# Performance work log

Hardware: AMD Instinct MI355X
Metric: run time of the kernel (lower is better)

Reference implementation:

```python
import jax, jax.numpy as jnp
import numpy as np

DIM = 192
HEADS = 4
EPS = 1e-12  # F.normalize default eps


def setup_inputs() -> dict:
    key = jax.random.key(0)
    ks = jax.random.split(key, 5)
    b, c, h, w = 8, DIM, 128, 128
    x = jax.random.normal(ks[0], (b, c, h, w), dtype=jnp.float32)
    w_qkv = jax.random.normal(ks[1], (3 * DIM, DIM, 1, 1), dtype=jnp.float32) * (1.0 / np.sqrt(DIM))
    w_dw = jax.random.normal(ks[2], (3 * DIM, 1, 3, 3), dtype=jnp.float32) * (1.0 / 3.0)
    w_proj = jax.random.normal(ks[3], (DIM, DIM, 1, 1), dtype=jnp.float32) * (1.0 / np.sqrt(DIM))
    temperature = jnp.ones((HEADS, 1, 1), dtype=jnp.float32)
    return {"x": x, "w_qkv": w_qkv, "w_dw": w_dw, "w_proj": w_proj, "temperature": temperature}


def _conv1x1(x, w):
    # x: [b,c,h,w], w: [o,c,1,1] -> [b,o,h,w]
    return jnp.einsum('bchw,oc->bohw', x, w[:, :, 0, 0])


def _dwconv3x3(x, w):
    # depthwise 3x3, padding=1; x: [b,C,h,w], w: [C,1,3,3]
    C = x.shape[1]
    return jax.lax.conv_general_dilated(
        x, w, window_strides=(1, 1), padding=((1, 1), (1, 1)),
        dimension_numbers=('NCHW', 'OIHW', 'NCHW'), feature_group_count=C)


def _l2norm(x):
    n = jnp.linalg.norm(x, axis=-1, keepdims=True)
    return x / jnp.maximum(n, EPS)


def reference(x, w_qkv, w_dw, w_proj, temperature):
    b, c, h, w = x.shape
    head = HEADS
    ch = c // head  # channels per head
    qkv = _dwconv3x3(_conv1x1(x, w_qkv), w_dw)  # [b, 3c, h, w]
    q, k, v = jnp.split(qkv, 3, axis=1)  # each [b, c, h, w]

    def to_heads(t):
        # b (head ch) h w -> b head h (ch w)
        t = t.reshape(b, head, ch, h, w)
        return t.transpose(0, 1, 3, 2, 4).reshape(b, head, h, ch * w)

    q1 = _l2norm(to_heads(q))
    k1 = _l2norm(to_heads(k))
    v1 = to_heads(v)
    # attn over height dim: [b, head, h, h]
    attn = jax.nn.softmax(jnp.einsum('bhif,bhjf->bhij', q1, k1) * temperature[None], axis=-1)
    out = jnp.einsum('bhij,bhjf->bhif', attn, v1)  # [b, head, h, ch*w]
    # b head h (ch w) -> b (head ch) h w
    out = out.reshape(b, head, h, ch, w).transpose(0, 1, 3, 2, 4).reshape(b, c, h, w)
    return _conv1x1(out, w_proj)
```

## Files before the change

kernel.cpp:

```cpp
#include <hip/hip_runtime.h>
#include <hip/hip_bf16.h>

#define BB 8
#define CC 192
#define C3 576
#define NH 4
#define CH 48
#define HH 128
#define WW 128
#define HW 16384
#define FF 6144

typedef short s16x8 __attribute__((ext_vector_type(8)));
typedef float f32x4 __attribute__((ext_vector_type(4)));

constexpr size_t SPM = 32ull * 128 * 128;

constexpr size_t OFF_XT  = 0;
constexpr size_t SZ_XT   = (size_t)BB * HW * CC * 2;
constexpr size_t OFF_WQ  = OFF_XT + SZ_XT;
constexpr size_t SZ_WQ   = (size_t)C3 * CC * 2;
constexpr size_t OFF_WP  = OFF_WQ + SZ_WQ;
constexpr size_t SZ_WP   = (size_t)CC * CC * 2;
constexpr size_t OFF_RAW = OFF_WP + SZ_WP;
constexpr size_t SZ_RAW  = (size_t)BB * C3 * HW * 2;
constexpr size_t OFF_DW  = OFF_RAW + SZ_RAW;
constexpr size_t OFF_SP  = OFF_DW + SZ_RAW;
constexpr size_t OFF_ATB = OFF_SP + 8 * SPM * 4;
constexpr size_t OFF_RQ  = OFF_ATB + 32ull * 128 * 128 * 2;
constexpr size_t OFF_RK  = OFF_RQ + 32 * 128 * 4;
constexpr size_t OFF_PS  = OFF_SP;

__device__ __forceinline__ short bf16bits(float v) {
  __hip_bfloat16 t = __float2bfloat16(v);
  return *reinterpret_cast<short*>(&t);
}
__device__ __forceinline__ float b2f(short u) {
  union { unsigned int i; float f; } x;
  x.i = ((unsigned int)(unsigned short)u) << 16;
  return x.f;
}

__device__ __forceinline__ void gload16(const void* g, void* l) {
  __builtin_amdgcn_global_load_lds((const __attribute__((address_space(1))) unsigned int*)g,
                                   (__attribute__((address_space(3))) unsigned int*)l, 16, 0, 0);
}

#define VMWAIT(N) asm volatile("s_waitcnt vmcnt(" #N ")" ::: "memory")
__device__ __forceinline__ void vmdrain() { asm volatile("s_waitcnt vmcnt(0)" ::: "memory"); }
__device__ __forceinline__ void ldsbar() {
  asm volatile("s_waitcnt lgkmcnt(0)" ::: "memory");
  __builtin_amdgcn_s_barrier();
}

__global__ __launch_bounds__(256) void k_cvt_t(const float* __restrict__ in,
                                               __hip_bfloat16* __restrict__ outT) {
  const int p0 = blockIdx.x * 64;
  const int c0 = blockIdx.y * 32;
  const int b = blockIdx.z;
  __shared__ float t[32][65];
  const float* ib = in + (size_t)b * CC * HW;
  const int tid = threadIdx.x;
  {
    const int c = tid >> 3, pl = (tid & 7) * 8;
    const float* s = ib + (size_t)(c0 + c) * HW + p0 + pl;
#pragma unroll
    for (int j = 0; j < 8; ++j) t[c][pl + j] = s[j];
  }
  __syncthreads();
  {
    const int pl = tid >> 2, cl = (tid & 3) * 8;
    __hip_bfloat16* d = outT + (size_t)b * HW * CC + (size_t)(p0 + pl) * CC + c0 + cl;
#pragma unroll
    for (int j = 0; j < 8; ++j) d[j] = __float2bfloat16(t[cl + j][pl]);
  }
}

__global__ __launch_bounds__(256) void k_cvt_w2(const float* __restrict__ in1, int n1,
                                                const float* __restrict__ in2, int n2,
                                                __hip_bfloat16* __restrict__ out) {
  const int i = blockIdx.x * 256 + threadIdx.x;
  if (i < n1) out[i] = __float2bfloat16(in1[i]);
  else if (i < n1 + n2) out[i] = __float2bfloat16(in2[i - n1]);
}

__global__ __launch_bounds__(256) void k_gemm(const __hip_bfloat16* __restrict__ xT,
                                              const __hip_bfloat16* __restrict__ Wb,
                                              __hip_bfloat16* __restrict__ out) {
  const int pG = blockIdx.x * 4;
  const int mBase = blockIdx.y * 96;
  const int b = blockIdx.z;
  __shared__ char smem[62976];
  const int tid = threadIdx.x, wave = tid >> 6, lane = tid & 63;
  const int wm = wave >> 1, wn = wave & 1;
  const __hip_bfloat16* xb = xT + (size_t)b * HW * CC;
  char* Bbase = smem + 36864;

#pragma unroll
  for (int it = 0; it < 9; ++it) {
    const int s = it * 256 + tid;
    const int kc = s / 384, ci = s % 384;
    const int row = ci & 15, kg = (ci >> 4) & 3, mf = ci >> 6;
    gload16(Wb + (size_t)(mBase + mf * 16 + row) * CC + kc * 32 + kg * 8,
            smem + it * 4096 + wave * 1024);
  }

  auto stageB = [&](int pt, int kc, int buf) {
    char* Blc = Bbase + buf * 8192;
    const int pBase = (pG + pt) * 128;
#pragma unroll
    for (int is = 0; is < 2; ++is) {
      const int ci = is * 256 + tid;
      const int col = ci & 15, kg = (ci >> 4) & 3, nf = ci >> 6;
      gload16(xb + (size_t)(pBase + nf * 16 + col) * CC + kc * 32 + kg * 8,
              Blc + is * 4096 + wave * 1024);
    }
  };

  short* E = (short*)Bbase;
  const int r0 = (lane >> 4) * 4, cl = lane & 15;

  for (int pt = 0; pt < 4; ++pt) {
    stageB(pt, 0, 0);
    stageB(pt, 1, 1);
    f32x4 acc[3][4] = {};
#pragma unroll
    for (int kc = 0; kc < 6; ++kc) {
      if (kc < 4) stageB(pt, kc + 2, (kc + 2) % 3);
      if (kc < 4) VMWAIT(4);
      else if (kc == 4) VMWAIT(2);
      else VMWAIT(0);
      __builtin_amdgcn_s_barrier();
      char* Alc = smem + kc * 6144;
      char* Blc = Bbase + (kc % 3) * 8192;
      s16x8 a[3], bf[4];
#pragma unroll
      for (int i = 0; i < 3; ++i) a[i] = *(const s16x8*)(Alc + ((wm * 3 + i) << 10) + (lane << 4));
#pragma unroll
      for (int j = 0; j < 4; ++j) bf[j] = *(const s16x8*)(Blc + ((wn * 4 + j) << 10) + (lane << 4));
#pragma unroll
      for (int i = 0; i < 3; ++i)
#pragma unroll
        for (int j = 0; j < 4; ++j)
          acc[i][j] = __builtin_amdgcn_mfma_f32_16x16x32_bf16(a[i], bf[j], acc[i][j], 0, 0, 0);
      __builtin_amdgcn_s_barrier();
    }
#pragma unroll
    for (int i = 0; i < 3; ++i) {
      const int lr = wm * 48 + i * 16 + r0;
#pragma unroll
      for (int j = 0; j < 4; ++j) {
        const int col = (wn * 4 + j) * 16 + cl;
#pragma unroll
        for (int r = 0; r < 4; ++r) E[(lr + r) * 136 + col] = bf16bits(acc[i][j][r]);
      }
    }
    ldsbar();
    __hip_bfloat16* ob = out + (size_t)b * C3 * HW + (pG + pt) * 128;
#pragma unroll
    for (int it = 0; it < 6; ++it) {
      const int vi = it * 256 + tid;
      const int row = vi >> 4, c8 = (vi & 15) * 8;
      const s16x8 v = *(const s16x8*)(E + row * 136 + c8);
      *(s16x8*)(ob + (size_t)(mBase + row) * HW + c8) = v;
    }
    ldsbar();
  }
}

__global__ __launch_bounds__(256) void k_dwconv(const __hip_bfloat16* __restrict__ in,
                                                const float* __restrict__ wdw,
                                                __hip_bfloat16* __restrict__ out,
                                                __hip_bfloat16* __restrict__ vt,
                                                float* __restrict__ psum) {
  const int h0 = blockIdx.x * 32;
  const int c = blockIdx.y;
  const int b = blockIdx.z;
  __shared__ __hip_bfloat16 IN[34][152];
  __shared__ char TR[8192];
  const int tid = threadIdx.x;
  const __hip_bfloat16* src = in + ((size_t)b * C3 + c) * HW;
  if (tid < 68) {
    const int r = tid >> 1, col = (tid & 1) ? 136 : 0;
    *(s16x8*)(&IN[r][col]) = (s16x8){};
  }
#pragma unroll
  for (int it = 0; it < 3; ++it) {
    const int vi = it * 256 + tid;
    if (vi < 544) {
      const int r = vi >> 4, w8 = vi & 15;
      const int hg = h0 - 1 + r;
      s16x8 v = {};
      if (hg >= 0 && hg < HH) v = *(const s16x8*)(src + (size_t)hg * WW + w8 * 8);
      *(s16x8*)(&IN[r][8 + w8 * 8]) = v;
    }
  }
  const float* wp = wdw + c * 9;
  float wgt[9];
#pragma unroll
  for (int q = 0; q < 9; ++q) wgt[q] = wp[q];
  __syncthreads();

  const int hl = tid >> 3, w0 = (tid & 7) * 16;
  float res[16] = {};
#pragma unroll
  for (int dh = 0; dh < 3; ++dh) {
    const __hip_bfloat16* rp = &IN[hl + dh][0];
    const s16x8 v0 = *(const s16x8*)(rp + w0);
    const s16x8 v1 = *(const s16x8*)(rp + w0 + 8);
    const s16x8 v2 = *(const s16x8*)(rp + w0 + 16);
    const s16x8 v3 = *(const s16x8*)(rp + w0 + 24);
    float rv[18];
    rv[0] = b2f(v0[7]);
#pragma unroll
    for (int e = 0; e < 8; ++e) rv[1 + e] = b2f(v1[e]);
#pragma unroll
    for (int e = 0; e < 8; ++e) rv[9 + e] = b2f(v2[e]);
    rv[17] = b2f(v3[0]);
    const float wa = wgt[dh * 3], wb = wgt[dh * 3 + 1], wc = wgt[dh * 3 + 2];
#pragma unroll
    for (int ww = 0; ww < 16; ++ww)
      res[ww] += rv[ww] * wa + rv[ww + 1] * wb + rv[ww + 2] * wc;
  }
  if (c < 2 * CC) {
    short pk[16];
#pragma unroll
    for (int ww = 0; ww < 16; ++ww) pk[ww] = bf16bits(res[ww]);
    __hip_bfloat16* dst = out + ((size_t)b * C3 + c) * HW + (size_t)(h0 + hl) * WW + w0;
    *(s16x8*)dst = *(const s16x8*)pk;
    *(s16x8*)(dst + 8) = *(const s16x8*)(pk + 8);
    float ss = 0.f;
#pragma unroll
    for (int ww = 0; ww < 16; ++ww) ss += res[ww] * res[ww];
#pragma unroll
    for (int off = 4; off > 0; off >>= 1) ss += __shfl_down(ss, off);
    if ((tid & 7) == 0) psum[((size_t)b * HH + h0 + hl) * 384 + c] = ss;
  } else {
    const int rel = c - 2 * CC;
    const int hd = rel / CH, ch = rel - hd * CH;
#pragma unroll
    for (int ww = 0; ww < 16; ++ww) {
      const int w = w0 + ww;
      const int blk = ((w << 2) + (hl >> 3)) ^ ((w >> 3) & 3);
      *(short*)(TR + (blk << 4) + ((hl & 7) << 1)) = bf16bits(res[ww]);
    }
    __syncthreads();
    const int w = tid >> 1, hf = tid & 1;
    short ot[16];
#pragma unroll
    for (int j = 0; j < 2; ++j) {
      const int hh = hf * 16 + j * 8;
      const int blk = ((w << 2) + (hh >> 3)) ^ ((w >> 3) & 3);
      *(s16x8*)(ot + j * 8) = *(const s16x8*)(TR + (blk << 4));
    }
    __hip_bfloat16* vd = vt + ((size_t)(b * NH + hd) * FF + (size_t)ch * WW + w) * HH + h0 + hf * 16;
    *(s16x8*)vd = *(const s16x8*)ot;
    *(s16x8*)(vd + 8) = *(const s16x8*)(ot + 8);
  }
}

__global__ __launch_bounds__(64) void k_norms2(const float* __restrict__ psum,
                                               float* __restrict__ rq, float* __restrict__ rk) {
  const int i = blockIdx.x;
  const int hd = blockIdx.y;
  const int b = blockIdx.z & 7;
  const int which = blockIdx.z >> 3;
  const int lane = threadIdx.x;
  float s = 0.f;
  if (lane < 48) s = psum[((size_t)b * HH + i) * 384 + which * CC + hd * CH + lane];
#pragma unroll
  for (int off = 32; off > 0; off >>= 1) s += __shfl_down(s, off);
  if (lane == 0) {
    const float n = sqrtf(s);
    float* dst = which ? rk : rq;
    dst[(b * NH + hd) * HH + i] = 1.f / fmaxf(n, 1e-12f);
  }
}

__global__ __launch_bounds__(256) void k_qkm(const __hip_bfloat16* __restrict__ dw,
                                             float* __restrict__ sp) {
  const int ks = blockIdx.x;
  const int bh = blockIdx.y;
  const int b = bh >> 2, hd = bh & 3;
  const __hip_bfloat16* qb = dw + ((size_t)b * C3 + hd * CH) * HW;
  const __hip_bfloat16* kb = dw + ((size_t)b * C3 + CC + hd * CH) * HW;
  __shared__ char smem[49152];
  const int tid = threadIdx.x, wave = tid >> 6, lane = tid & 63;
  const int wm = wave >> 1, wn = wave & 1;
  f32x4 acc[4][4] = {};

  auto stage = [&](int chunk, int buf) {
    const int ch = ks * 6 + (chunk >> 2);
    const int w0 = (chunk & 3) * 32;
    char* Alc = smem + buf * 16384;
    char* Blc = Alc + 8192;
#pragma unroll
    for (int is = 0; is < 2; ++is) {
      const int ci = is * 256 + tid;
      const int row = ci & 15, kg = (ci >> 4) & 3, mf = ci >> 6;
      gload16(qb + (size_t)ch * HW + (mf * 16 + row) * WW + w0 + kg * 8,
              Alc + is * 4096 + wave * 1024);
    }
#pragma unroll
    for (int is = 0; is < 2; ++is) {
      const int ci = is * 256 + tid;
      const int col = ci & 15, kg = (ci >> 4) & 3, nf = ci >> 6;
      gload16(kb + (size_t)ch * HW + (nf * 16 + col) * WW + w0 + kg * 8,
              Blc + is * 4096 + wave * 1024);
    }
  };

  stage(0, 0);
  stage(1, 1);
  for (int chunk = 0; chunk < 24; ++chunk) {
    if (chunk < 22) stage(chunk + 2, (chunk + 2) % 3);
    if (chunk < 22) VMWAIT(8);
    else if (chunk == 22) VMWAIT(4);
    else VMWAIT(0);
    __builtin_amdgcn_s_barrier();
    char* Alc = smem + (chunk % 3) * 16384;
    char* Blc = Alc + 8192;
    s16x8 a[4], bf[4];
#pragma unroll
    for (int i = 0; i < 4; ++i) a[i] = *(const s16x8*)(Alc + ((wm * 4 + i) << 10) + (lane << 4));
#pragma unroll
    for (int j = 0; j < 4; ++j) bf[j] = *(const s16x8*)(Blc + ((wn * 4 + j) << 10) + (lane << 4));
#pragma unroll
    for (int i = 0; i < 4; ++i)
#pragma unroll
      for (int j = 0; j < 4; ++j)
        acc[i][j] = __builtin_amdgcn_mfma_f32_16x16x32_bf16(a[i], bf[j], acc[i][j], 0, 0, 0);
    __builtin_amdgcn_s_barrier();
  }
  float* o = sp + (size_t)ks * SPM + (size_t)bh * HH * HH;
  const int r0 = (lane >> 4) * 4, cl = lane & 15;
#pragma unroll
  for (int i = 0; i < 4; ++i)
#pragma unroll
    for (int j = 0; j < 4; ++j) {
      const int ii = wm * 64 + i * 16 + r0;
      const int jj = wn * 64 + j * 16 + cl;
#pragma unroll
      for (int r = 0; r < 4; ++r) o[(ii + r) * HH + jj] = acc[i][j][r];
    }
}

__global__ __launch_bounds__(256) void k_softmax(const float* __restrict__ sp,
                                                 const float* __restrict__ rq,
                                                 const float* __restrict__ rk,
                                                 const float* __restrict__ temp,
                                                 __hip_bfloat16* __restrict__ atb) {
  const int wave = threadIdx.x >> 6, lane = threadIdx.x & 63;
  const int i = blockIdx.x * 4 + wave;
  const int bh = blockIdx.y;
  const int hd = bh & 3;
  const size_t rowoff = ((size_t)bh * HH + i) * HH;
  float s0 = 0.f, s1 = 0.f;
#pragma unroll
  for (int ks = 0; ks < 8; ++ks) {
    s0 += sp[ks * SPM + rowoff + lane];
    s1 += sp[ks * SPM + rowoff + lane + 64];
  }
  const float scale = rq[bh * HH + i] * temp[hd];
  s0 *= scale * rk[bh * HH + lane];
  s1 *= scale * rk[bh * HH + lane + 64];
  float m = fmaxf(s0, s1);
#pragma unroll
  for (int off = 32; off > 0; off >>= 1) m = fmaxf(m, __shfl_xor(m, off));
  const float e0 = expf(s0 - m), e1 = expf(s1 - m);
  float ssum = e0 + e1;
#pragma unroll
  for (int off = 32; off > 0; off >>= 1) ssum += __shfl_xor(ssum, off);
  const float inv = 1.f / ssum;
  atb[rowoff + lane] = __float2bfloat16(e0 * inv);
  atb[rowoff + lane + 64] = __float2bfloat16(e1 * inv);
}

__global__ __launch_bounds__(256) void k_pvm(const __hip_bfloat16* __restrict__ atb,
                                             const __hip_bfloat16* __restrict__ vt,
                                             __hip_bfloat16* __restrict__ pvout) {
  const int fs0 = blockIdx.x * 2;
  const int bh = blockIdx.y;
  const __hip_bfloat16* ab = atb + (size_t)bh * HH * HH;
  __shared__ char smem[57344];
  const int tid = threadIdx.x, wave = tid >> 6, lane = tid & 63;
  const int wm = wave >> 1, wn = wave & 1;

#pragma unroll
  for (int it = 0; it < 8; ++it) {
    const int s = it * 256 + tid;
    const int kc = s >> 9, ci = s & 511;
    const int row = ci & 15, kg = (ci >> 4) & 3, mf = ci >> 6;
    gload16(ab + (size_t)(mf * 16 + row) * HH + kc * 32 + kg * 8,
            smem + it * 4096 + wave * 1024);
  }
  char* Bbase = smem + 32768;

  auto stageB = [&](int st, int buf) {
    const int fs = fs0 + (st >> 2);
    const int kj0 = (st & 3) * 32;
    const __hip_bfloat16* vb = vt + ((size_t)bh * FF + fs * 128) * HH;
    char* Blc = Bbase + buf * 8192;
#pragma unroll
    for (int is = 0; is < 2; ++is) {
      const int ci = is * 256 + tid;
      const int col = ci & 15, kg = (ci >> 4) & 3, nf = ci >> 6;
      gload16(vb + (size_t)(nf * 16 + col) * HH + kj0 + kg * 8,
              Blc + is * 4096 + wave * 1024);
    }
  };

  stageB(0, 0);
  stageB(1, 1);
  const int r0 = (lane >> 4) * 4, cl = lane & 15;
  for (int fr = 0; fr < 2; ++fr) {
    f32x4 acc[4][4] = {};
#pragma unroll
    for (int kc = 0; kc < 4; ++kc) {
      const int st = fr * 4 + kc;
      if (st < 6) stageB(st + 2, (st + 2) % 3);
      if (st < 6) VMWAIT(4);
      else if (st == 6) VMWAIT(2);
      else VMWAIT(0);
      __builtin_amdgcn_s_barrier();
      char* Alc = smem + kc * 8192;
      char* Blc = Bbase + (st % 3) * 8192;
      s16x8 a[4], bf[4];
#pragma unroll
      for (int i = 0; i < 4; ++i) a[i] = *(const s16x8*)(Alc + ((wm * 4 + i) << 10) + (lane << 4));
#pragma unroll
      for (int j = 0; j < 4; ++j) bf[j] = *(const s16x8*)(Blc + ((wn * 4 + j) << 10) + (lane << 4));
#pragma unroll
      for (int i = 0; i < 4; ++i)
#pragma unroll
        for (int j = 0; j < 4; ++j)
          acc[i][j] = __builtin_amdgcn_mfma_f32_16x16x32_bf16(a[i], bf[j], acc[i][j], 0, 0, 0);
      __builtin_amdgcn_s_barrier();
    }
    __hip_bfloat16* ob = pvout + (size_t)bh * HH * FF;
    const int fs = fs0 + fr;
#pragma unroll
    for (int i = 0; i < 4; ++i)
#pragma unroll
      for (int j = 0; j < 4; ++j) {
        const int ii = wm * 64 + i * 16 + r0;
        const int f = fs * 128 + (wn * 4 + j) * 16 + cl;
#pragma unroll
        for (int r = 0; r < 4; ++r) ob[(size_t)(ii + r) * FF + f] = __float2bfloat16(acc[i][j][r]);
      }
  }
}

__global__ __launch_bounds__(256) void k_proj(const __hip_bfloat16* __restrict__ pv,
                                              const __hip_bfloat16* __restrict__ Wp,
                                              float* __restrict__ out) {
  const int i = blockIdx.x;
  const int b = blockIdx.y;
  __shared__ __hip_bfloat16 Al[6144];
  __shared__ __hip_bfloat16 Braw[12288];
  __shared__ __hip_bfloat16 Bfrag[4096];
  char* Alc = (char*)Al;
  char* Brc = (char*)Braw;
  char* Bfc = (char*)Bfrag;
  const int tid = threadIdx.x, wave = tid >> 6, lane = tid & 63;
  const int wm = wave >> 1, wn = wave & 1;
  f32x4 acc[6][4] = {};
  for (int hf = 0; hf < 2; ++hf) {
    if (hf) __syncthreads();
#pragma unroll
    for (int it = 0; it < 6; ++it) {
      const int vi = it * 256 + tid;
      const int r = vi >> 4, w8 = vi & 15;
      const int hi = (r >= 48) ? 1 : 0;
      const int hd = hf * 2 + hi, ch = r - hi * 48;
      const s16x8 v = *(const s16x8*)(pv + ((size_t)(b * NH + hd) * HH + i) * FF + ch * 128 + w8 * 8);
      *(s16x8*)(Brc + r * 256 + ((w8 ^ (r & 15)) << 4)) = v;
    }
    __syncthreads();
    for (int kc = 0; kc < 3; ++kc) {
      const int c0 = hf * 96 + kc * 32;
#pragma unroll
      for (int is = 0; is < 3; ++is) {
        const int ci = is * 256 + tid;
        const int row = ci & 15, kg = (ci >> 4) & 3, mf = ci >> 6;
        gload16(Wp + (size_t)(mf * 16 + row) * CC + c0 + kg * 8,
                Alc + is * 4096 + wave * 1024);
      }
#pragma unroll
      for (int it = 0; it < 2; ++it) {
        const int vi = it * 256 + tid;
        const int col = vi & 15, kg = (vi >> 4) & 3, nf = vi >> 6;
        const int w = nf * 16 + col;
        short tmp[8];
#pragma unroll
        for (int e = 0; e < 8; ++e) {
          const int r = (kc * 4 + kg) * 8 + e;
          tmp[e] = *(const short*)(Brc + r * 256 + (((w >> 3) ^ (r & 15)) << 4) + (w & 7) * 2);
        }
        *(s16x8*)(Bfc + ((nf * 64 + kg * 16 + col) << 4)) = *(const s16x8*)tmp;
      }
      vmdrain();
      __syncthreads();
      s16x8 a[6], bf[4];
#pragma unroll
      for (int mi = 0; mi < 6; ++mi)
        a[mi] = *(const s16x8*)(Alc + ((wm * 6 + mi) << 10) + (lane << 4));
#pragma unroll
      for (int j = 0; j < 4; ++j)
        bf[j] = *(const s16x8*)(Bfc + (((wn * 4 + j) * 64 + lane) << 4));
#pragma unroll
      for (int mi = 0; mi < 6; ++mi)
#pragma unroll
        for (int j = 0; j < 4; ++j)
          acc[mi][j] = __builtin_amdgcn_mfma_f32_16x16x32_bf16(a[mi], bf[j], acc[mi][j], 0, 0, 0);
      __syncthreads();
    }
  }
  const int r0 = (lane >> 4) * 4, cl = lane & 15;
#pragma unroll
  for (int mi = 0; mi < 6; ++mi) {
    const int o = (wm * 6 + mi) * 16 + r0;
#pragma unroll
    for (int j = 0; j < 4; ++j) {
      const int w = (wn * 4 + j) * 16 + cl;
      float* dst = out + ((size_t)b * CC + o) * HW + i * 128 + w;
#pragma unroll
      for (int r = 0; r < 4; ++r) dst[(size_t)r * HW] = acc[mi][j][r];
    }
  }
}

extern "C" void kernel_launch(void* const* d_in, const int* in_sizes, int n_in,
                              void* d_out, int out_size, void* d_ws, size_t ws_size,
                              hipStream_t stream) {
  const float* x     = (const float*)d_in[0];
  const float* wqkv  = (const float*)d_in[1];
  const float* wdw   = (const float*)d_in[2];
  const float* wproj = (const float*)d_in[3];
  const float* temp  = (const float*)d_in[4];

  char* ws = (char*)d_ws;
  __hip_bfloat16* xTb    = (__hip_bfloat16*)(ws + OFF_XT);
  __hip_bfloat16* vt     = (__hip_bfloat16*)(ws + OFF_XT);
  __hip_bfloat16* Wq     = (__hip_bfloat16*)(ws + OFF_WQ);
  __hip_bfloat16* Wp     = (__hip_bfloat16*)(ws + OFF_WP);
  __hip_bfloat16* qkvraw = (__hip_bfloat16*)(ws + OFF_RAW);
  __hip_bfloat16* pvout  = (__hip_bfloat16*)(ws + OFF_RAW);
  __hip_bfloat16* qkvdw  = (__hip_bfloat16*)(ws + OFF_DW);
  float* sp    = (float*)(ws + OFF_SP);
  float* psum  = (float*)(ws + OFF_PS);
  __hip_bfloat16* atb = (__hip_bfloat16*)(ws + OFF_ATB);
  float* rq    = (float*)(ws + OFF_RQ);
  float* rk    = (float*)(ws + OFF_RK);

  k_cvt_w2<<<dim3((C3 * CC + CC * CC + 255) / 256), 256, 0, stream>>>(wqkv, C3 * CC, wproj, CC * CC, Wq);
  k_cvt_t<<<dim3(HW / 64, CC / 32, BB), 256, 0, stream>>>(x, xTb);
  k_gemm<<<dim3(HW / 512, C3 / 96, BB), 256, 0, stream>>>(xTb, Wq, qkvraw);
  k_dwconv<<<dim3(HH / 32, C3, BB), 256, 0, stream>>>(qkvraw, wdw, qkvdw, vt, psum);
  k_norms2<<<dim3(HH, NH, 2 * BB), 64, 0, stream>>>(psum, rq, rk);
  k_qkm<<<dim3(8, 32), 256, 0, stream>>>(qkvdw, sp);
  k_softmax<<<dim3(HH / 4, 32), 256, 0, stream>>>(sp, rq, rk, temp, atb);
  k_pvm<<<dim3(24, 32), 256, 0, stream>>>(atb, vt, pvout);
  k_proj<<<dim3(HH, BB), 256, 0, stream>>>(pvout, Wp, (float*)d_out);
}
```

Measured before the change: 253.3 us.

## Loop dwconv over height tiles with register prefetch; split QK^T GEMM rows

The depthwise conv kernel now processes all four 32-row height tiles of a channel in one block, double-buffering shared memory and prefetching the next tile into registers while computing the current one. It launches 4x fewer blocks and overlaps global loads with compute. The QK^T kernel is split along the query-row dimension into two 64-row halves, which doubles its grid from 256 to 512 blocks and shrinks per-block LDS and accumulators for better occupancy. The trade-off is reduced parallelism in dwconv and duplicated K loads in qkm.

```diff
diff --git a/kernel.cpp b/kernel.cpp
--- a/kernel.cpp
+++ b/kernel.cpp
@@ -173,89 +173,116 @@
                                                 __hip_bfloat16* __restrict__ out,
                                                 __hip_bfloat16* __restrict__ vt,
                                                 float* __restrict__ psum) {
-  const int h0 = blockIdx.x * 32;
-  const int c = blockIdx.y;
+  const int c = blockIdx.x;
   const int b = blockIdx.z;
-  __shared__ __hip_bfloat16 IN[34][152];
+  __shared__ __hip_bfloat16 IN[2][34][152];
   __shared__ char TR[8192];
   const int tid = threadIdx.x;
   const __hip_bfloat16* src = in + ((size_t)b * C3 + c) * HW;
-  if (tid < 68) {
-    const int r = tid >> 1, col = (tid & 1) ? 136 : 0;
-    *(s16x8*)(&IN[r][col]) = (s16x8){};
-  }
-#pragma unroll
-  for (int it = 0; it < 3; ++it) {
-    const int vi = it * 256 + tid;
-    if (vi < 544) {
-      const int r = vi >> 4, w8 = vi & 15;
-      const int hg = h0 - 1 + r;
-      s16x8 v = {};
-      if (hg >= 0 && hg < HH) v = *(const s16x8*)(src + (size_t)hg * WW + w8 * 8);
-      *(s16x8*)(&IN[r][8 + w8 * 8]) = v;
-    }
+  const bool isV = (c >= 2 * CC);
+  if (tid < 136) {
+    const int bz = tid >= 68, t2 = tid - bz * 68;
+    const int r = t2 >> 1, col = (t2 & 1) ? 136 : 0;
+    *(s16x8*)(&IN[bz][r][col]) = (s16x8){};
   }
   const float* wp = wdw + c * 9;
   float wgt[9];
 #pragma unroll
   for (int q = 0; q < 9; ++q) wgt[q] = wp[q];
+
+  s16x8 ld[3];
+  auto loadTile = [&](int h0) {
+#pragma unroll
+    for (int it = 0; it < 3; ++it) {
+      const int vi = it * 256 + tid;
+      if (vi < 544) {
+        const int r = vi >> 4, w8 = vi & 15;
+        const int hg = h0 - 1 + r;
+        s16x8 v = {};
+        if (hg >= 0 && hg < HH) v = *(const s16x8*)(src + (size_t)hg * WW + w8 * 8);
+        ld[it] = v;
+      }
+    }
+  };
+  auto writeTile = [&](int buf) {
+#pragma unroll
+    for (int it = 0; it < 3; ++it) {
+      const int vi = it * 256 + tid;
+      if (vi < 544) {
+        const int r = vi >> 4, w8 = vi & 15;
+        *(s16x8*)(&IN[buf][r][8 + w8 * 8]) = ld[it];
+      }
+    }
+  };
+
+  loadTile(0);
+  writeTile(0);
   __syncthreads();
 
   const int hl = tid >> 3, w0 = (tid & 7) * 16;
-  float res[16] = {};
-#pragma unroll
-  for (int dh = 0; dh < 3; ++dh) {
-    const __hip_bfloat16* rp = &IN[hl + dh][0];
-    const s16x8 v0 = *(const s16x8*)(rp + w0);
-    const s16x8 v1 = *(const s16x8*)(rp + w0 + 8);
-    const s16x8 v2 = *(const s16x8*)(rp + w0 + 16);
-    const s16x8 v3 = *(const s16x8*)(rp + w0 + 24);
-    float rv[18];
-    rv[0] = b2f(v0[7]);
-#pragma unroll
-    for (int e = 0; e < 8; ++e) rv[1 + e] = b2f(v1[e]);
-#pragma unroll
-    for (int e = 0; e < 8; ++e) rv[9 + e] = b2f(v2[e]);
-    rv[17] = b2f(v3[0]);
-    const float wa = wgt[dh * 3], wb = wgt[dh * 3 + 1], wc = wgt[dh * 3 + 2];
-#pragma unroll
-    for (int ww = 0; ww < 16; ++ww)
-      res[ww] += rv[ww] * wa + rv[ww + 1] * wb + rv[ww + 2] * wc;
-  }
-  if (c < 2 * CC) {
-    short pk[16];
-#pragma unroll
-    for (int ww = 0; ww < 16; ++ww) pk[ww] = bf16bits(res[ww]);
-    __hip_bfloat16* dst = out + ((size_t)b * C3 + c) * HW + (size_t)(h0 + hl) * WW + w0;
-    *(s16x8*)dst = *(const s16x8*)pk;
-    *(s16x8*)(dst + 8) = *(const s16x8*)(pk + 8);
-    float ss = 0.f;
-#pragma unroll
-    for (int ww = 0; ww < 16; ++ww) ss += res[ww] * res[ww];
-#pragma unroll
-    for (int off = 4; off > 0; off >>= 1) ss += __shfl_down(ss, off);
-    if ((tid & 7) == 0) psum[((size_t)b * HH + h0 + hl) * 384 + c] = ss;
-  } else {
-    const int rel = c - 2 * CC;
-    const int hd = rel / CH, ch = rel - hd * CH;
-#pragma unroll
-    for (int ww = 0; ww < 16; ++ww) {
-      const int w = w0 + ww;
-      const int blk = ((w << 2) + (hl >> 3)) ^ ((w >> 3) & 3);
-      *(short*)(TR + (blk << 4) + ((hl & 7) << 1)) = bf16bits(res[ww]);
-    }
-    __syncthreads();
-    const int w = tid >> 1, hf = tid & 1;
-    short ot[16];
-#pragma unroll
-    for (int j = 0; j < 2; ++j) {
-      const int hh = hf * 16 + j * 8;
-      const int blk = ((w << 2) + (hh >> 3)) ^ ((w >> 3) & 3);
-      *(s16x8*)(ot + j * 8) = *(const s16x8*)(TR + (blk << 4));
-    }
-    __hip_bfloat16* vd = vt + ((size_t)(b * NH + hd) * FF + (size_t)ch * WW + w) * HH + h0 + hf * 16;
-    *(s16x8*)vd = *(const s16x8*)ot;
-    *(s16x8*)(vd + 8) = *(const s16x8*)(ot + 8);
+  for (int t = 0; t < 4; ++t) {
+    const int h0 = t * 32;
+    const int cur = t & 1;
+    if (t < 3) loadTile(h0 + 32);
+    float res[16] = {};
+#pragma unroll
+    for (int dh = 0; dh < 3; ++dh) {
+      const __hip_bfloat16* rp = &IN[cur][hl + dh][0];
+      const s16x8 v0 = *(const s16x8*)(rp + w0);
+      const s16x8 v1 = *(const s16x8*)(rp + w0 + 8);
+      const s16x8 v2 = *(const s16x8*)(rp + w0 + 16);
+      const s16x8 v3 = *(const s16x8*)(rp + w0 + 24);
+      float rv[18];
+      rv[0] = b2f(v0[7]);
+#pragma unroll
+      for (int e = 0; e < 8; ++e) rv[1 + e] = b2f(v1[e]);
+#pragma unroll
+      for (int e = 0; e < 8; ++e) rv[9 + e] = b2f(v2[e]);
+      rv[17] = b2f(v3[0]);
+      const float wa = wgt[dh * 3], wb = wgt[dh * 3 + 1], wc = wgt[dh * 3 + 2];
+#pragma unroll
+      for (int ww = 0; ww < 16; ++ww)
+        res[ww] += rv[ww] * wa + rv[ww + 1] * wb + rv[ww + 2] * wc;
+    }
+    if (!isV) {
+      short pk[16];
+#pragma unroll
+      for (int ww = 0; ww < 16; ++ww) pk[ww] = bf16bits(res[ww]);
+      __hip_bfloat16* dst = out + ((size_t)b * C3 + c) * HW + (size_t)(h0 + hl) * WW + w0;
+      *(s16x8*)dst = *(const s16x8*)pk;
+      *(s16x8*)(dst + 8) = *(const s16x8*)(pk + 8);
+      float ss = 0.f;
+#pragma unroll
+      for (int ww = 0; ww < 16; ++ww) ss += res[ww] * res[ww];
+#pragma unroll
+      for (int off = 4; off > 0; off >>= 1) ss += __shfl_down(ss, off);
+      if ((tid & 7) == 0) psum[((size_t)b * HH + h0 + hl) * 384 + c] = ss;
+      if (t < 3) writeTile(cur ^ 1);
+      __syncthreads();
+    } else {
+      const int rel = c - 2 * CC;
+      const int hd = rel / CH, ch = rel - hd * CH;
+#pragma unroll
+      for (int ww = 0; ww < 16; ++ww) {
+        const int w = w0 + ww;
+        const int blk = ((w << 2) + (hl >> 3)) ^ ((w >> 3) & 3);
+        *(short*)(TR + (blk << 4) + ((hl & 7) << 1)) = bf16bits(res[ww]);
+      }
+      __syncthreads();
+      const int w = tid >> 1, hf = tid & 1;
+      short ot[16];
+#pragma unroll
+      for (int j = 0; j < 2; ++j) {
+        const int hh = hf * 16 + j * 8;
+        const int blk = ((w << 2) + (hh >> 3)) ^ ((w >> 3) & 3);
+        *(s16x8*)(ot + j * 8) = *(const s16x8*)(TR + (blk << 4));
+      }
+      __hip_bfloat16* vd = vt + ((size_t)(b * NH + hd) * FF + (size_t)ch * WW + w) * HH + h0 + hf * 16;
+      *(s16x8*)vd = *(const s16x8*)ot;
+      *(s16x8*)(vd + 8) = *(const s16x8*)(ot + 8);
+      if (t < 3) writeTile(cur ^ 1);
+      __syncthreads();
+    }
   }
 }
 
@@ -281,25 +308,24 @@
                                              float* __restrict__ sp) {
   const int ks = blockIdx.x;
   const int bh = blockIdx.y;
+  const int i0 = blockIdx.z * 64;
   const int b = bh >> 2, hd = bh & 3;
   const __hip_bfloat16* qb = dw + ((size_t)b * C3 + hd * CH) * HW;
   const __hip_bfloat16* kb = dw + ((size_t)b * C3 + CC + hd * CH) * HW;
-  __shared__ char smem[49152];
+  __shared__ char smem[36864];
   const int tid = threadIdx.x, wave = tid >> 6, lane = tid & 63;
   const int wm = wave >> 1, wn = wave & 1;
-  f32x4 acc[4][4] = {};
+  f32x4 acc[2][4] = {};
 
   auto stage = [&](int chunk, int buf) {
     const int ch = ks * 6 + (chunk >> 2);
     const int w0 = (chunk & 3) * 32;
-    char* Alc = smem + buf * 16384;
-    char* Blc = Alc + 8192;
-#pragma unroll
-    for (int is = 0; is < 2; ++is) {
-      const int ci = is * 256 + tid;
-      const int row = ci & 15, kg = (ci >> 4) & 3, mf = ci >> 6;
-      gload16(qb + (size_t)ch * HW + (mf * 16 + row) * WW + w0 + kg * 8,
-              Alc + is * 4096 + wave * 1024);
+    char* Alc = smem + buf * 12288;
+    char* Blc = Alc + 4096;
+    {
+      const int row = tid & 15, kg = (tid >> 4) & 3;
+      gload16(qb + (size_t)ch * HW + (i0 + (tid >> 6) * 16 + row) * WW + w0 + kg * 8,
+              Alc + wave * 1024);
     }
 #pragma unroll
     for (int is = 0; is < 2; ++is) {
@@ -314,19 +340,19 @@
   stage(1, 1);
   for (int chunk = 0; chunk < 24; ++chunk) {
     if (chunk < 22) stage(chunk + 2, (chunk + 2) % 3);
-    if (chunk < 22) VMWAIT(8);
-    else if (chunk == 22) VMWAIT(4);
+    if (chunk < 22) VMWAIT(6);
+    else if (chunk == 22) VMWAIT(3);
     else VMWAIT(0);
     __builtin_amdgcn_s_barrier();
-    char* Alc = smem + (chunk % 3) * 16384;
-    char* Blc = Alc + 8192;
-    s16x8 a[4], bf[4];
-#pragma unroll
-    for (int i = 0; i < 4; ++i) a[i] = *(const s16x8*)(Alc + ((wm * 4 + i) << 10) + (lane << 4));
+    char* Alc = smem + (chunk % 3) * 12288;
+    char* Blc = Alc + 4096;
+    s16x8 a[2], bf[4];
+#pragma unroll
+    for (int i = 0; i < 2; ++i) a[i] = *(const s16x8*)(Alc + ((wm * 2 + i) << 10) + (lane << 4));
 #pragma unroll
     for (int j = 0; j < 4; ++j) bf[j] = *(const s16x8*)(Blc + ((wn * 4 + j) << 10) + (lane << 4));
 #pragma unroll
-    for (int i = 0; i < 4; ++i)
+    for (int i = 0; i < 2; ++i)
 #pragma unroll
       for (int j = 0; j < 4; ++j)
         acc[i][j] = __builtin_amdgcn_mfma_f32_16x16x32_bf16(a[i], bf[j], acc[i][j], 0, 0, 0);
@@ -335,10 +361,10 @@
   float* o = sp + (size_t)ks * SPM + (size_t)bh * HH * HH;
   const int r0 = (lane >> 4) * 4, cl = lane & 15;
 #pragma unroll
-  for (int i = 0; i < 4; ++i)
+  for (int i = 0; i < 2; ++i)
 #pragma unroll
     for (int j = 0; j < 4; ++j) {
-      const int ii = wm * 64 + i * 16 + r0;
+      const int ii = i0 + wm * 32 + i * 16 + r0;
       const int jj = wn * 64 + j * 16 + cl;
 #pragma unroll
       for (int r = 0; r < 4; ++r) o[(ii + r) * HH + jj] = acc[i][j][r];
@@ -556,9 +582,9 @@
   k_cvt_w2<<<dim3((C3 * CC + CC * CC + 255) / 256), 256, 0, stream>>>(wqkv, C3 * CC, wproj, CC * CC, Wq);
   k_cvt_t<<<dim3(HW / 64, CC / 32, BB), 256, 0, stream>>>(x, xTb);
   k_gemm<<<dim3(HW / 512, C3 / 96, BB), 256, 0, stream>>>(xTb, Wq, qkvraw);
-  k_dwconv<<<dim3(HH / 32, C3, BB), 256, 0, stream>>>(qkvraw, wdw, qkvdw, vt, psum);
+  k_dwconv<<<dim3(C3, 1, BB), 256, 0, stream>>>(qkvraw, wdw, qkvdw, vt, psum);
   k_norms2<<<dim3(HH, NH, 2 * BB), 64, 0, stream>>>(psum, rq, rk);
-  k_qkm<<<dim3(8, 32), 256, 0, stream>>>(qkvdw, sp);
+  k_qkm<<<dim3(8, 32, 2), 256, 0, stream>>>(qkvdw, sp);
   k_softmax<<<dim3(HH / 4, 32), 256, 0, stream>>>(sp, rq, rk, temp, atb);
   k_pvm<<<dim3(24, 32), 256, 0, stream>>>(atb, vt, pvout);
   k_proj<<<dim3(HH, BB), 256, 0, stream>>>(pvout, Wp, (float*)d_out);
```

New measurement: 259.2 us. 1.02x slower.
